# Performance work log

Measured on AMD Instinct MI355X. Metric: run time of the kernel, lower is better.

The kernel has to match this reference:

```python
import jax, jax.numpy as jnp
import numpy as np

NEG_SLOPE = 0.2

def setup_inputs() -> dict:
    key = jax.random.key(0)
    k1, k2, k3 = jax.random.split(key, 3)
    x = jax.random.normal(k1, (4, 4096, 64), dtype=jnp.float32)
    weight_key = jax.random.normal(k2, (64, 1), dtype=jnp.float32)
    weight_query = jax.random.normal(k3, (64, 1), dtype=jnp.float32)
    return {"x": x, "weight_key": weight_key, "weight_query": weight_query}

def reference(x, weight_key, weight_query):
    # x: [bz, N, F]; key/query: [bz, N, 1]
    k = jnp.matmul(x, weight_key)          # [bz, N, 1]
    q = jnp.matmul(x, weight_query)        # [bz, N, 1]
    # additive broadcast attention: scores[b,i,j] = k[b,i] + q[b,j]
    scores = k + jnp.swapaxes(q, 1, 2)     # [bz, N, N]
    scores = jax.nn.leaky_relu(scores, negative_slope=NEG_SLOPE)
    attention = jax.nn.softmax(scores, axis=2)
    # dropout is identity in eval mode
    attn_feat = jnp.matmul(attention, x)   # [bz, N, F]
    return jnp.transpose(attn_feat, (0, 2, 1))  # [bz, F, N]
```

## Files before the change

### kernel.cpp

```cpp
#include <hip/hip_runtime.h>

#define N 4096
#define F 64
#define BZ 4
#define MAGIC1 0x1F2E3D4Cu
#define MAGIC2 0x5A6B7C8Du

#define ALOAD(p)     __hip_atomic_load((p),  __ATOMIC_RELAXED, __HIP_MEMORY_SCOPE_AGENT)
#define ASTORE(p, v) __hip_atomic_store((p), (v), __ATOMIC_RELAXED, __HIP_MEMORY_SCOPE_AGENT)

__device__ __forceinline__ unsigned int f2ord(float f) {
    unsigned int u = __float_as_uint(f);
    return (u & 0x80000000u) ? ~u : (u ^ 0x80000000u);
}
__device__ __forceinline__ float ord2f(unsigned int v) {
    unsigned int b = (v & 0x80000000u) ? (v ^ 0x80000000u) : ~v;
    return __uint_as_float(b);
}

__device__ __forceinline__ void batch_barrier(unsigned* bflags, unsigned* bdone,
                                              unsigned magic, int chunk,
                                              int tid, int wave, int lane) {
    __syncthreads();
    if (tid == 0) ASTORE(bflags + chunk, magic);
    if (chunk == 0) {
        if (wave == 0) {
            for (;;) {
                unsigned a = ALOAD(bflags + lane);
                if (__all(a == magic)) break;
                __builtin_amdgcn_s_sleep(2);
            }
            if (lane == 0) ASTORE(bdone, magic);
        }
    } else {
        if (wave == 0 && lane == 0) {
            while (ALOAD(bdone) != magic) __builtin_amdgcn_s_sleep(2);
        }
    }
    __syncthreads();
    asm volatile("" ::: "memory");
}

__global__ __launch_bounds__(1024) void fused_gat(
        const float* __restrict__ x, const float* __restrict__ wk,
        const float* __restrict__ wq, unsigned* __restrict__ flags1,
        unsigned* __restrict__ flags2, unsigned* __restrict__ done1,
        unsigned* __restrict__ done2,
        unsigned long long* __restrict__ qkey,
        unsigned long long* __restrict__ skey,
        unsigned long long* __restrict__ kp,
        float* __restrict__ out) {
    __shared__ __align__(16) char smem[66432];
    const int bid = blockIdx.x;
    const int tid = threadIdx.x;
    const int wave = tid >> 6, lane = tid & 63;
    const int b = bid >> 6, chunk = bid & 63;
    unsigned* bf1 = flags1 + (b << 8);
    unsigned* bf2 = flags2 + (b << 8);
    unsigned* bd1 = done1 + (b << 6);
    unsigned* bd2 = done2 + (b << 6);

    float* kks = (float*)(smem + 36864);

    {
        const int row = tid >> 4;
        const int fq = tid & 15;
        const int grow = (chunk << 6) + row;
        const int f0 = fq << 2;
        float4 xv = *(const float4*)(x + ((size_t)b * N + grow) * F + f0);
        float4 k4 = *(const float4*)(wk + f0);
        float4 q4 = *(const float4*)(wq + f0);
        float kk = xv.x * k4.x + xv.y * k4.y + xv.z * k4.z + xv.w * k4.w;
        float qq = xv.x * q4.x + xv.y * q4.y + xv.z * q4.z + xv.w * q4.w;
#pragma unroll
        for (int off = 1; off <= 8; off <<= 1) {
            kk += __shfl_xor(kk, off, 16);
            qq += __shfl_xor(qq, off, 16);
        }
        if (fq == 0) {
            kks[row] = kk;
            ASTORE(qkey + b * N + grow,
                   ((unsigned long long)f2ord(qq) << 32) | (unsigned int)grow);
        }
    }
    batch_barrier(bf1, bd1, MAGIC1, chunk, tid, wave, lane);

    {
        unsigned long long* qs = (unsigned long long*)smem;
        unsigned short (*pc)[64] = (unsigned short(*)[64])(smem + 32768);
        unsigned short (*pc2)[64] = (unsigned short(*)[64])(smem + 34816);
        const ulonglong2* qb2 = (const ulonglong2*)(qkey + b * N);
        ulonglong2* qs2 = (ulonglong2*)qs;
        qs2[tid] = qb2[tid];
        qs2[tid + 1024] = qb2[tid + 1024];
        const float kk = kks[lane];
        const unsigned int thetaOrd = f2ord(-kk);
        __syncthreads();

        const unsigned long long myKey = qs[(chunk << 6) + lane];
        int cnt = 0, cnt2 = 0;
        const ulonglong2* q2 = (const ulonglong2*)qs;
        const int s0 = wave * 128;
#pragma unroll 8
        for (int t2 = 0; t2 < 128; ++t2) {
            ulonglong2 v = q2[s0 + t2];
            cnt  += (int)(v.x < myKey) + (int)(v.y < myKey);
            cnt2 += (int)((unsigned int)(v.x >> 32) < thetaOrd)
                  + (int)((unsigned int)(v.y >> 32) < thetaOrd);
        }
        pc[wave][lane]  = (unsigned short)cnt;
        pc2[wave][lane] = (unsigned short)cnt2;
        __syncthreads();

        if (wave == 0) {
            int r = 0, p = 0;
#pragma unroll
            for (int w = 0; w < 16; ++w) { r += pc[w][lane]; p += pc2[w][lane]; }
            ASTORE(skey + b * N + r, myKey);
            ASTORE(kp + b * N + (chunk << 6) + lane,
                   ((unsigned long long)__float_as_uint(kk) << 32)
                 | (unsigned int)p);
        }
    }
    batch_barrier(bf2, bd2, MAGIC2, chunk, tid, wave, lane);

    {
        const int f = ((chunk & 7) << 3) | (chunk >> 3);
        float* SUF1 = (float*)smem;
        float* PRE2 = (float*)(smem + 16416);
        float* SUFD = (float*)(smem + 32832);
        float* PRED = (float*)(smem + 49248);
        float* wt1  = (float*)(smem + 65664);
        float* wtd1 = (float*)(smem + 65728);
        float* wt2  = (float*)(smem + 65792);
        float* wtd2 = (float*)(smem + 65856);
        float* wb1  = (float*)(smem + 65920);
        float* wbd1 = (float*)(smem + 65984);
        float* wb2  = (float*)(smem + 66048);
        float* wbd2 = (float*)(smem + 66112);
        float* QmaxS = (float*)(smem + 66176);
        const int t0 = tid << 2;

        if (tid == 0)
            QmaxS[0] = ord2f((unsigned int)(skey[b * N + N - 1] >> 32));
        __syncthreads();
        const float Qmax = QmaxS[0];

        ulonglong2 s01 = *(const ulonglong2*)(skey + b * N + t0);
        ulonglong2 s23 = *(const ulonglong2*)(skey + b * N + t0 + 2);
        ulonglong2 k01 = *(const ulonglong2*)(kp + b * N + t0);
        ulonglong2 k23 = *(const ulonglong2*)(kp + b * N + t0 + 2);
        unsigned long long sk[4] = {s01.x, s01.y, s23.x, s23.y};
        unsigned long long kv[4] = {k01.x, k01.y, k23.x, k23.y};
        float e1[4], e2[4], w1[4], w2[4];
        const float* xbf = x + (size_t)b * N * F + f;
#pragma unroll
        for (int r = 0; r < 4; ++r) {
            float qv = ord2f((unsigned int)(sk[r] >> 32));
            unsigned ia = (unsigned int)sk[r] & (N - 1);
            float d = qv - Qmax;
            e1[r] = __expf(d);
            e2[r] = __expf(0.2f * d);
            float xf = xbf[(size_t)ia * F];
            w1[r] = e1[r] * xf;
            w2[r] = e2[r] * xf;
        }

        float lp2_0 = 0.f, lp2_1 = w2[0], lp2_2 = lp2_1 + w2[1], lp2_3 = lp2_2 + w2[2];
        float T2 = lp2_3 + w2[3];
        float lpd_0 = 0.f, lpd_1 = e2[0], lpd_2 = lpd_1 + e2[1], lpd_3 = lpd_2 + e2[2];
        float TD2 = lpd_3 + e2[3];
        float ls1_3 = w1[3], ls1_2 = w1[2] + ls1_3, ls1_1 = w1[1] + ls1_2, ls1_0 = w1[0] + ls1_1;
        float T1 = ls1_0;
        float lsd_3 = e1[3], lsd_2 = e1[2] + lsd_3, lsd_1 = e1[1] + lsd_2, lsd_0 = e1[0] + lsd_1;
        float TD1 = lsd_0;

        float ip2 = T2, ipd2 = TD2;
#pragma unroll
        for (int d = 1; d < 64; d <<= 1) {
            float n1 = __shfl_up(ip2, d, 64);
            float n2 = __shfl_up(ipd2, d, 64);
            if (lane >= d) { ip2 += n1; ipd2 += n2; }
        }
        float is1 = T1, isd1 = TD1;
#pragma unroll
        for (int d = 1; d < 64; d <<= 1) {
            float n1 = __shfl_down(is1, d, 64);
            float n2 = __shfl_down(isd1, d, 64);
            if (lane + d < 64) { is1 += n1; isd1 += n2; }
        }
        if (lane == 63) { wt2[wave] = ip2; wtd2[wave] = ipd2; }
        if (lane == 0)  { wt1[wave] = is1; wtd1[wave] = isd1; }
        __syncthreads();
        if (wave == 0 && lane < 16) {
            float v = wt2[lane], vd = wtd2[lane];
            float s = v, sd = vd;
#pragma unroll
            for (int d = 1; d < 16; d <<= 1) {
                float n1 = __shfl_up(s, d, 64);
                float n2 = __shfl_up(sd, d, 64);
                if (lane >= d) { s += n1; sd += n2; }
            }
            wb2[lane] = s - v; wbd2[lane] = sd - vd;
            if (lane == 15) { PRE2[N] = s; PRED[N] = sd; }
        }
        if (wave == 1 && lane < 16) {
            float v = wt1[lane], vd = wtd1[lane];
            float s = v, sd = vd;
#pragma unroll
            for (int d = 1; d < 16; d <<= 1) {
                float n1 = __shfl_down(s, d, 64);
                float n2 = __shfl_down(sd, d, 64);
                if (lane + d < 16) { s += n1; sd += n2; }
            }
            wb1[lane] = s - v; wbd1[lane] = sd - vd;
            if (lane == 0) { SUF1[N] = 0.f; SUFD[N] = 0.f; }
        }
        __syncthreads();
        float bp2 = wb2[wave] + (ip2 - T2);
        float bpd = wbd2[wave] + (ipd2 - TD2);
        float bs1 = wb1[wave] + (is1 - T1);
        float bsd = wbd1[wave] + (isd1 - TD1);
        float4 o;
        o.x = bp2 + lp2_0; o.y = bp2 + lp2_1; o.z = bp2 + lp2_2; o.w = bp2 + lp2_3;
        *(float4*)(PRE2 + t0) = o;
        o.x = bpd + lpd_0; o.y = bpd + lpd_1; o.z = bpd + lpd_2; o.w = bpd + lpd_3;
        *(float4*)(PRED + t0) = o;
        o.x = bs1 + ls1_0; o.y = bs1 + ls1_1; o.z = bs1 + ls1_2; o.w = bs1 + ls1_3;
        *(float4*)(SUF1 + t0) = o;
        o.x = bsd + lsd_0; o.y = bsd + lsd_1; o.z = bsd + lsd_2; o.w = bsd + lsd_3;
        *(float4*)(SUFD + t0) = o;
        __syncthreads();

        float ra[4];
#pragma unroll
        for (int r = 0; r < 4; ++r) {
            float kk = __uint_as_float((unsigned int)(kv[r] >> 32));
            int p = (int)(kv[r] & 0xFFFFFFFFu);
            if ((unsigned)p > N) p = N;
            float u = kk + Qmax;
            float M = fmaxf(u, 0.2f * u);
            float c1 = __expf(u - M);
            float c2 = __expf(0.2f * u - M);
            float num = c1 * SUF1[p] + c2 * PRE2[p];
            float den = c1 * SUFD[p] + c2 * PRED[p];
            ra[r] = num / den;
        }
        float4 res; res.x = ra[0]; res.y = ra[1]; res.z = ra[2]; res.w = ra[3];
        *(float4*)(out + ((size_t)(b * F + f)) * N + t0) = res;
    }
}

extern "C" void kernel_launch(void* const* d_in, const int* in_sizes, int n_in,
                              void* d_out, int out_size, void* d_ws, size_t ws_size,
                              hipStream_t stream) {
    const float* x  = (const float*)d_in[0];
    const float* wk = (const float*)d_in[1];
    const float* wq = (const float*)d_in[2];
    float* out = (float*)d_out;

    unsigned* wsu = (unsigned*)d_ws;
    unsigned* flags1 = wsu;
    unsigned* flags2 = flags1 + 4 * 256;
    unsigned* done1  = flags2 + 4 * 256;
    unsigned* done2  = done1 + 4 * 64;
    unsigned long long* qkey = (unsigned long long*)(done2 + 4 * 64 + 64);
    unsigned long long* skey = qkey + BZ * N;
    unsigned long long* kp   = skey + BZ * N;

    fused_gat<<<BZ * 64, 1024, 0, stream>>>(x, wk, wq, flags1, flags2,
                                            done1, done2, qkey, skey, kp, out);
}
```

Before: 79.72 us.

## Compute Qmax locally, split barrier to overlap exp work, scatter sorted values in LDS

Each block now computes Qmax with a wave/block max reduction over the q keys it already loads into LDS, so it no longer reads the last sorted key from global memory. The second grid barrier is split: a block posts its arrival flag, computes the x loads and exponentials for its own rows, and only then waits. After the barrier it scatters those values into LDS by rank instead of gathering sorted keys and x values from global memory. Rank and threshold counts are packed into one 32-bit word per row, which shrinks the global traffic between phases. The packed field allows 13 bits for the count, which holds for N=4096.

```diff
diff --git a/kernel.cpp b/kernel.cpp
--- a/kernel.cpp
+++ b/kernel.cpp
@@ -16,6 +16,9 @@
 __device__ __forceinline__ float ord2f(unsigned int v) {
     unsigned int b = (v & 0x80000000u) ? (v ^ 0x80000000u) : ~v;
     return __uint_as_float(b);
+}
+__device__ __forceinline__ unsigned umax2(unsigned a, unsigned b) {
+    return a > b ? a : b;
 }
 
 __device__ __forceinline__ void batch_barrier(unsigned* bflags, unsigned* bdone,
@@ -45,10 +48,8 @@
         const float* __restrict__ x, const float* __restrict__ wk,
         const float* __restrict__ wq, unsigned* __restrict__ flags1,
         unsigned* __restrict__ flags2, unsigned* __restrict__ done1,
-        unsigned* __restrict__ done2,
-        unsigned long long* __restrict__ qkey,
-        unsigned long long* __restrict__ skey,
-        unsigned long long* __restrict__ kp,
+        unsigned* __restrict__ done2, float* __restrict__ karr,
+        unsigned long long* __restrict__ qkey, unsigned* __restrict__ prA,
         float* __restrict__ out) {
     __shared__ __align__(16) char smem[66432];
     const int bid = blockIdx.x;
@@ -60,7 +61,12 @@
     unsigned* bd1 = done1 + (b << 6);
     unsigned* bd2 = done2 + (b << 6);
 
-    float* kks = (float*)(smem + 36864);
+    unsigned long long* qs = (unsigned long long*)smem;
+    unsigned short (*pc)[64]  = (unsigned short(*)[64])(smem + 32768);
+    unsigned short (*pc2)[64] = (unsigned short(*)[64])(smem + 34816);
+    float* kks      = (float*)(smem + 36864);
+    unsigned* wmaxU = (unsigned*)(smem + 37120);
+    float* QmaxS    = (float*)(smem + 37184);
 
     {
         const int row = tid >> 4;
@@ -79,6 +85,7 @@
         }
         if (fq == 0) {
             kks[row] = kk;
+            ASTORE(karr + b * N + grow, kk);
             ASTORE(qkey + b * N + grow,
                    ((unsigned long long)f2ord(qq) << 32) | (unsigned int)grow);
         }
@@ -86,13 +93,18 @@
     batch_barrier(bf1, bd1, MAGIC1, chunk, tid, wave, lane);
 
     {
-        unsigned long long* qs = (unsigned long long*)smem;
-        unsigned short (*pc)[64] = (unsigned short(*)[64])(smem + 32768);
-        unsigned short (*pc2)[64] = (unsigned short(*)[64])(smem + 34816);
         const ulonglong2* qb2 = (const ulonglong2*)(qkey + b * N);
         ulonglong2* qs2 = (ulonglong2*)qs;
-        qs2[tid] = qb2[tid];
-        qs2[tid + 1024] = qb2[tid + 1024];
+        ulonglong2 v0 = qb2[tid];
+        ulonglong2 v1 = qb2[tid + 1024];
+        qs2[tid] = v0;
+        qs2[tid + 1024] = v1;
+        unsigned mh = umax2(umax2((unsigned)(v0.x >> 32), (unsigned)(v0.y >> 32)),
+                            umax2((unsigned)(v1.x >> 32), (unsigned)(v1.y >> 32)));
+#pragma unroll
+        for (int off = 1; off < 64; off <<= 1)
+            mh = umax2(mh, (unsigned)__shfl_xor((int)mh, off, 64));
+        if (lane == 0) wmaxU[wave] = mh;
         const float kk = kks[lane];
         const unsigned int thetaOrd = f2ord(-kk);
         __syncthreads();
@@ -116,16 +128,62 @@
             int r = 0, p = 0;
 #pragma unroll
             for (int w = 0; w < 16; ++w) { r += pc[w][lane]; p += pc2[w][lane]; }
-            ASTORE(skey + b * N + r, myKey);
-            ASTORE(kp + b * N + (chunk << 6) + lane,
-                   ((unsigned long long)__float_as_uint(kk) << 32)
-                 | (unsigned int)p);
-        }
-    }
-    batch_barrier(bf2, bd2, MAGIC2, chunk, tid, wave, lane);
+            ASTORE(prA + b * N + (chunk << 6) + lane,
+                   (((unsigned)p) << 16) | (unsigned)r);
+            unsigned m2 = wmaxU[lane & 15];
+#pragma unroll
+            for (int off = 1; off < 16; off <<= 1)
+                m2 = umax2(m2, (unsigned)__shfl_xor((int)m2, off, 16));
+            if (lane == 0) QmaxS[0] = ord2f(m2);
+        }
+    }
+
+    __syncthreads();
+    if (tid == 0) ASTORE(bf2 + chunk, MAGIC2);
+
+    const int f = ((chunk & 7) << 3) | (chunk >> 3);
+    const int t0 = tid << 2;
+    const float Qmax = QmaxS[0];
+    const float* xp = x + ((size_t)b * N + t0) * F + f;
+    float xf0 = xp[0], xf1 = xp[F], xf2 = xp[2 * F], xf3 = xp[3 * F];
+    float4 kqv = *(const float4*)(karr + b * N + t0);
+    ulonglong2 qA = ((const ulonglong2*)qs)[t0 >> 1];
+    ulonglong2 qB = ((const ulonglong2*)qs)[(t0 >> 1) + 1];
+    float d0 = ord2f((unsigned)(qA.x >> 32)) - Qmax;
+    float d1 = ord2f((unsigned)(qA.y >> 32)) - Qmax;
+    float d2 = ord2f((unsigned)(qB.x >> 32)) - Qmax;
+    float d3 = ord2f((unsigned)(qB.y >> 32)) - Qmax;
+    float e1_0 = __expf(d0), e1_1 = __expf(d1), e1_2 = __expf(d2), e1_3 = __expf(d3);
+    float e2_0 = __expf(0.2f * d0), e2_1 = __expf(0.2f * d1);
+    float e2_2 = __expf(0.2f * d2), e2_3 = __expf(0.2f * d3);
+    float w1_0 = e1_0 * xf0, w1_1 = e1_1 * xf1, w1_2 = e1_2 * xf2, w1_3 = e1_3 * xf3;
+    float w2_0 = e2_0 * xf0, w2_1 = e2_1 * xf1, w2_2 = e2_2 * xf2, w2_3 = e2_3 * xf3;
+    float u0 = kqv.x + Qmax, u1 = kqv.y + Qmax, u2 = kqv.z + Qmax, u3 = kqv.w + Qmax;
+    float M0 = fmaxf(u0, 0.2f * u0), M1 = fmaxf(u1, 0.2f * u1);
+    float M2 = fmaxf(u2, 0.2f * u2), M3 = fmaxf(u3, 0.2f * u3);
+    float c1_0 = __expf(u0 - M0), c1_1 = __expf(u1 - M1);
+    float c1_2 = __expf(u2 - M2), c1_3 = __expf(u3 - M3);
+    float c2_0 = __expf(0.2f * u0 - M0), c2_1 = __expf(0.2f * u1 - M1);
+    float c2_2 = __expf(0.2f * u2 - M2), c2_3 = __expf(0.2f * u3 - M3);
+
+    if (chunk == 0) {
+        if (wave == 0) {
+            for (;;) {
+                unsigned a = ALOAD(bf2 + lane);
+                if (__all(a == MAGIC2)) break;
+                __builtin_amdgcn_s_sleep(2);
+            }
+            if (lane == 0) ASTORE(bd2, MAGIC2);
+        }
+    } else {
+        if (wave == 0 && lane == 0) {
+            while (ALOAD(bd2) != MAGIC2) __builtin_amdgcn_s_sleep(2);
+        }
+    }
+    __syncthreads();
+    asm volatile("" ::: "memory");
 
     {
-        const int f = ((chunk & 7) << 3) | (chunk >> 3);
         float* SUF1 = (float*)smem;
         float* PRE2 = (float*)(smem + 16416);
         float* SUFD = (float*)(smem + 32832);
@@ -138,41 +196,33 @@
         float* wbd1 = (float*)(smem + 65984);
         float* wb2  = (float*)(smem + 66048);
         float* wbd2 = (float*)(smem + 66112);
-        float* QmaxS = (float*)(smem + 66176);
-        const int t0 = tid << 2;
-
-        if (tid == 0)
-            QmaxS[0] = ord2f((unsigned int)(skey[b * N + N - 1] >> 32));
-        __syncthreads();
-        const float Qmax = QmaxS[0];
-
-        ulonglong2 s01 = *(const ulonglong2*)(skey + b * N + t0);
-        ulonglong2 s23 = *(const ulonglong2*)(skey + b * N + t0 + 2);
-        ulonglong2 k01 = *(const ulonglong2*)(kp + b * N + t0);
-        ulonglong2 k23 = *(const ulonglong2*)(kp + b * N + t0 + 2);
-        unsigned long long sk[4] = {s01.x, s01.y, s23.x, s23.y};
-        unsigned long long kv[4] = {k01.x, k01.y, k23.x, k23.y};
-        float e1[4], e2[4], w1[4], w2[4];
-        const float* xbf = x + (size_t)b * N * F + f;
-#pragma unroll
-        for (int r = 0; r < 4; ++r) {
-            float qv = ord2f((unsigned int)(sk[r] >> 32));
-            unsigned ia = (unsigned int)sk[r] & (N - 1);
-            float d = qv - Qmax;
-            e1[r] = __expf(d);
-            e2[r] = __expf(0.2f * d);
-            float xf = xbf[(size_t)ia * F];
-            w1[r] = e1[r] * xf;
-            w2[r] = e2[r] * xf;
-        }
-
-        float lp2_0 = 0.f, lp2_1 = w2[0], lp2_2 = lp2_1 + w2[1], lp2_3 = lp2_2 + w2[2];
-        float T2 = lp2_3 + w2[3];
-        float lpd_0 = 0.f, lpd_1 = e2[0], lpd_2 = lpd_1 + e2[1], lpd_3 = lpd_2 + e2[2];
-        float TD2 = lpd_3 + e2[3];
-        float ls1_3 = w1[3], ls1_2 = w1[2] + ls1_3, ls1_1 = w1[1] + ls1_2, ls1_0 = w1[0] + ls1_1;
+
+        uint4 pv4 = *(const uint4*)(prA + b * N + t0);
+        unsigned rk0 = pv4.x & 4095u, rk1 = pv4.y & 4095u;
+        unsigned rk2 = pv4.z & 4095u, rk3 = pv4.w & 4095u;
+        int p0 = (int)((pv4.x >> 16) & 0x1FFFu); if (p0 > N) p0 = N;
+        int p1 = (int)((pv4.y >> 16) & 0x1FFFu); if (p1 > N) p1 = N;
+        int p2 = (int)((pv4.z >> 16) & 0x1FFFu); if (p2 > N) p2 = N;
+        int p3 = (int)((pv4.w >> 16) & 0x1FFFu); if (p3 > N) p3 = N;
+
+        SUF1[rk0] = w1_0; SUF1[rk1] = w1_1; SUF1[rk2] = w1_2; SUF1[rk3] = w1_3;
+        PRE2[rk0] = w2_0; PRE2[rk1] = w2_1; PRE2[rk2] = w2_2; PRE2[rk3] = w2_3;
+        SUFD[rk0] = e1_0; SUFD[rk1] = e1_1; SUFD[rk2] = e1_2; SUFD[rk3] = e1_3;
+        PRED[rk0] = e2_0; PRED[rk1] = e2_1; PRED[rk2] = e2_2; PRED[rk3] = e2_3;
+        __syncthreads();
+
+        float4 rw1 = *(const float4*)(SUF1 + t0);
+        float4 rw2 = *(const float4*)(PRE2 + t0);
+        float4 re1 = *(const float4*)(SUFD + t0);
+        float4 re2 = *(const float4*)(PRED + t0);
+
+        float lp2_0 = 0.f, lp2_1 = rw2.x, lp2_2 = lp2_1 + rw2.y, lp2_3 = lp2_2 + rw2.z;
+        float T2 = lp2_3 + rw2.w;
+        float lpd_0 = 0.f, lpd_1 = re2.x, lpd_2 = lpd_1 + re2.y, lpd_3 = lpd_2 + re2.z;
+        float TD2 = lpd_3 + re2.w;
+        float ls1_3 = rw1.w, ls1_2 = rw1.z + ls1_3, ls1_1 = rw1.y + ls1_2, ls1_0 = rw1.x + ls1_1;
         float T1 = ls1_0;
-        float lsd_3 = e1[3], lsd_2 = e1[2] + lsd_3, lsd_1 = e1[1] + lsd_2, lsd_0 = e1[0] + lsd_1;
+        float lsd_3 = re1.w, lsd_2 = re1.z + lsd_3, lsd_1 = re1.y + lsd_2, lsd_0 = re1.x + lsd_1;
         float TD1 = lsd_0;
 
         float ip2 = T2, ipd2 = TD2;
@@ -232,21 +282,11 @@
         *(float4*)(SUFD + t0) = o;
         __syncthreads();
 
-        float ra[4];
-#pragma unroll
-        for (int r = 0; r < 4; ++r) {
-            float kk = __uint_as_float((unsigned int)(kv[r] >> 32));
-            int p = (int)(kv[r] & 0xFFFFFFFFu);
-            if ((unsigned)p > N) p = N;
-            float u = kk + Qmax;
-            float M = fmaxf(u, 0.2f * u);
-            float c1 = __expf(u - M);
-            float c2 = __expf(0.2f * u - M);
-            float num = c1 * SUF1[p] + c2 * PRE2[p];
-            float den = c1 * SUFD[p] + c2 * PRED[p];
-            ra[r] = num / den;
-        }
-        float4 res; res.x = ra[0]; res.y = ra[1]; res.z = ra[2]; res.w = ra[3];
+        float4 res;
+        res.x = (c1_0 * SUF1[p0] + c2_0 * PRE2[p0]) / (c1_0 * SUFD[p0] + c2_0 * PRED[p0]);
+        res.y = (c1_1 * SUF1[p1] + c2_1 * PRE2[p1]) / (c1_1 * SUFD[p1] + c2_1 * PRED[p1]);
+        res.z = (c1_2 * SUF1[p2] + c2_2 * PRE2[p2]) / (c1_2 * SUFD[p2] + c2_2 * PRED[p2]);
+        res.w = (c1_3 * SUF1[p3] + c2_3 * PRE2[p3]) / (c1_3 * SUFD[p3] + c2_3 * PRED[p3]);
         *(float4*)(out + ((size_t)(b * F + f)) * N + t0) = res;
     }
 }
@@ -261,13 +301,13 @@
 
     unsigned* wsu = (unsigned*)d_ws;
     unsigned* flags1 = wsu;
-    unsigned* flags2 = flags1 + 4 * 256;
-    unsigned* done1  = flags2 + 4 * 256;
-    unsigned* done2  = done1 + 4 * 64;
-    unsigned long long* qkey = (unsigned long long*)(done2 + 4 * 64 + 64);
-    unsigned long long* skey = qkey + BZ * N;
-    unsigned long long* kp   = skey + BZ * N;
+    unsigned* flags2 = wsu + 1024;
+    unsigned* done1  = wsu + 2048;
+    unsigned* done2  = wsu + 2304;
+    float* karr = (float*)(wsu + 2624);
+    unsigned long long* qkey = (unsigned long long*)(wsu + 19008);
+    unsigned* prA = wsu + 51776;
 
     fused_gat<<<BZ * 64, 1024, 0, stream>>>(x, wk, wq, flags1, flags2,
-                                            done1, done2, qkey, skey, kp, out);
-}
+                                            done1, done2, karr, qkey, prA, out);
+}
```

New measurement: 79.19 us. Within noise of the previous version (-0.7%).
